# Kernel optimization log

Hardware: AMD Instinct MI355X
Metric: run time of the kernel (lower is better)

Reference implementation:

```python
import jax, jax.numpy as jnp
import numpy as np

C = 384
NH = 8        # LocalCrossAttention heads
CA_NH = 2     # inner CrossAttention heads
D_WIN = 6
SIGMA = D_WIN / 2.0
EPS = 1e-6


def _ln(x, g, b):
    mu = jnp.mean(x, axis=-1, keepdims=True)
    var = jnp.mean((x - mu) ** 2, axis=-1, keepdims=True)
    return (x - mu) / jnp.sqrt(var + EPS) * g + b


def _cross_attn(qx, kvx, Wq, Wkv, Wp, bp, nh):
    B, QN, c = qx.shape
    N = kvx.shape[1]
    hd = c // nh
    scale = hd ** -0.5
    qh = (qx @ Wq).reshape(B, QN, nh, hd).transpose(0, 2, 1, 3) * scale  # bhqd
    kvh = (kvx @ Wkv).reshape(B, N, 2, nh, hd).transpose(2, 0, 3, 1, 4)
    k, v = kvh[0], kvh[1]                                               # bhkd
    attn = jax.nn.softmax(jnp.einsum('bhqd,bhkd->bhqk', qh, k), axis=-1)
    x = jnp.einsum('bhqk,bhkd->bhqd', attn, v).transpose(0, 2, 1, 3).reshape(B, QN, c)
    return x @ Wp + bp


def _forward(q, kv, Wq, Wkv, Wproj, bproj, Wp_w, Wp_b, vp_w, vp_b, qpos_w, qpos_b,
             ca1_Wq, ca1_Wkv, ca1_Wproj, ca1_bproj,
             ca2_Wq, ca2_Wkv, ca2_Wproj, ca2_bproj,
             lnq1_g, lnq1_b, lnkv1_g, lnkv1_b, lnq2_g, lnq2_b, lnkv2_g, lnkv2_b, H, W):
    bs, QN, c = q.shape
    N = kv.shape[1]
    hd = c // NH
    scale = hd ** -0.5

    # main q/k/v
    qh = (q @ Wq).reshape(bs, QN, NH, hd).transpose(0, 2, 1, 3) * scale   # [bs,NH,QN,hd]
    kvh = (kv @ Wkv).reshape(bs, N, 2, NH, hd).transpose(2, 0, 3, 1, 4)
    k, v = kvh[0], kvh[1]                                                 # [bs,NH,N,hd]

    # position prediction branch
    q_for_pos = jnp.tile(q, (1, H, 1))                                    # [bs,QN*H,C]
    p = q_for_pos @ qpos_w + qpos_b
    p = _cross_attn(_ln(p, lnq1_g, lnq1_b), _ln(q_for_pos, lnkv1_g, lnkv1_b),
                    ca1_Wq, ca1_Wkv, ca1_Wproj, ca1_bproj, CA_NH)
    p = _cross_attn(_ln(p, lnq2_g, lnq2_b), _ln(kv, lnkv2_g, lnkv2_b),
                    ca2_Wq, ca2_Wkv, ca2_Wproj, ca2_bproj, CA_NH)
    p_t = jax.nn.sigmoid(jnp.tanh(p @ Wp_w + Wp_b) @ vp_w + vp_b) * W     # [bs,QN*H,1]

    # Gaussian window over W columns, broadcast over heads
    idx = jnp.arange(W, dtype=q.dtype)                                    # [W]
    gauss = jnp.exp(-((idx[None, :] - p_t) ** 2) / (2.0 * SIGMA ** 2))    # [bs,QN*H,W]
    gauss = gauss[:, None]                                                # [bs,1,QN*H,W]

    attn = jnp.einsum('bhqd,bhkd->bhqk', qh, k)                           # [bs,NH,QN,N]
    attn = attn.reshape(bs, NH, QN * H, W) * gauss
    attn = attn.reshape(bs, NH, QN, N)
    attn = jax.nn.softmax(attn, axis=-1)

    x = jnp.einsum('bhqk,bhkd->bhqd', attn, v).transpose(0, 2, 1, 3).reshape(bs, QN, c)
    return x @ Wproj + bproj


def setup_inputs() -> dict:
    key = jax.random.key(0)
    ks = jax.random.split(key, 16)
    s = 0.05
    d = {
        'q': jax.random.normal(ks[0], (32, 64, C), jnp.float32),
        'kv': jax.random.normal(ks[1], (32, 1024, C), jnp.float32),
        'Wq': jax.random.normal(ks[2], (C, C), jnp.float32) * s,
        'Wkv': jax.random.normal(ks[3], (C, 2 * C), jnp.float32) * s,
        'Wproj': jax.random.normal(ks[4], (C, C), jnp.float32) * s,
        'bproj': jnp.zeros((C,), jnp.float32),
        'Wp_w': jax.random.normal(ks[5], (C, C), jnp.float32) * s,
        'Wp_b': jnp.zeros((C,), jnp.float32),
        'vp_w': jax.random.normal(ks[6], (C, 1), jnp.float32) * s,
        'vp_b': jnp.zeros((1,), jnp.float32),
        'qpos_w': jax.random.normal(ks[7], (C, C), jnp.float32) * s,
        'qpos_b': jnp.zeros((C,), jnp.float32),
        'ca1_Wq': jax.random.normal(ks[8], (C, C), jnp.float32) * s,
        'ca1_Wkv': jax.random.normal(ks[9], (C, 2 * C), jnp.float32) * s,
        'ca1_Wproj': jax.random.normal(ks[10], (C, C), jnp.float32) * s,
        'ca1_bproj': jnp.zeros((C,), jnp.float32),
        'ca2_Wq': jax.random.normal(ks[11], (C, C), jnp.float32) * s,
        'ca2_Wkv': jax.random.normal(ks[12], (C, 2 * C), jnp.float32) * s,
        'ca2_Wproj': jax.random.normal(ks[13], (C, C), jnp.float32) * s,
        'ca2_bproj': jnp.zeros((C,), jnp.float32),
        'lnq1_g': jnp.ones((C,), jnp.float32), 'lnq1_b': jnp.zeros((C,), jnp.float32),
        'lnkv1_g': jnp.ones((C,), jnp.float32), 'lnkv1_b': jnp.zeros((C,), jnp.float32),
        'lnq2_g': jnp.ones((C,), jnp.float32), 'lnq2_b': jnp.zeros((C,), jnp.float32),
        'lnkv2_g': jnp.ones((C,), jnp.float32), 'lnkv2_b': jnp.zeros((C,), jnp.float32),
        'H': 8,
        'W': 128,
    }
    return d


def reference(q, kv, Wq, Wkv, Wproj, bproj, Wp_w, Wp_b, vp_w, vp_b, qpos_w, qpos_b,
              ca1_Wq, ca1_Wkv, ca1_Wproj, ca1_bproj,
              ca2_Wq, ca2_Wkv, ca2_Wproj, ca2_bproj,
              lnq1_g, lnq1_b, lnkv1_g, lnkv1_b, lnq2_g, lnq2_b, lnkv2_g, lnkv2_b, H, W):
    return _forward(q, kv, Wq, Wkv, Wproj, bproj, Wp_w, Wp_b, vp_w, vp_b, qpos_w, qpos_b,
                    ca1_Wq, ca1_Wkv, ca1_Wproj, ca1_bproj,
                    ca2_Wq, ca2_Wkv, ca2_Wproj, ca2_bproj,
                    lnq1_g, lnq1_b, lnkv1_g, lnkv1_b, lnq2_g, lnq2_b, lnkv2_g, lnkv2_b, H, W)
```

## Files before the change

kernel.cpp:

```cpp
#include <hip/hip_runtime.h>
#include <math.h>

#define MFMA __builtin_amdgcn_mfma_f32_16x16x32_bf16
typedef __attribute__((ext_vector_type(8))) short bf16x8;
typedef __attribute__((ext_vector_type(4))) float f32x4;
typedef unsigned short ushort_t;

__device__ __forceinline__ unsigned short tbf_hi(float x) {
    return (unsigned short)(__float_as_uint(x) >> 16);
}
__device__ __forceinline__ unsigned short tbf_lo(float x) {
    unsigned u = __float_as_uint(x);
    float r = x - __uint_as_float(u & 0xFFFF0000u);
    return (unsigned short)(__float_as_uint(r) >> 16);
}
__device__ __forceinline__ unsigned packhi(unsigned u0, unsigned u1) {
#if __has_builtin(__builtin_amdgcn_perm)
    return __builtin_amdgcn_perm(u1, u0, 0x07060302u);
#else
    return (u1 & 0xFFFF0000u) | (u0 >> 16);
#endif
}
__device__ __forceinline__ void tsplit8(const float* v, unsigned* hw, unsigned* lw) {
#pragma unroll
    for (int t = 0; t < 4; ++t) {
        unsigned u0 = __float_as_uint(v[2 * t]);
        unsigned u1 = __float_as_uint(v[2 * t + 1]);
        float r0 = v[2 * t]     - __uint_as_float(u0 & 0xFFFF0000u);
        float r1 = v[2 * t + 1] - __uint_as_float(u1 & 0xFFFF0000u);
        hw[t] = packhi(u0, u1);
        lw[t] = packhi(__float_as_uint(r0), __float_as_uint(r1));
    }
}

#if __has_builtin(__builtin_amdgcn_global_load_lds)
#define HAVE_GLDS 1
__device__ __forceinline__ void gld16(const ushort_t* g, ushort_t* l) {
    __builtin_amdgcn_global_load_lds(
        (const __attribute__((address_space(1))) unsigned int*)g,
        (__attribute__((address_space(3))) unsigned int*)l, 16, 0, 0);
}
#else
#define HAVE_GLDS 0
#endif

__global__ __launch_bounds__(256) void ln_stats_kernel(
    const float* __restrict__ src, float* __restrict__ mu,
    float* __restrict__ rs, int rows) {
    int row = blockIdx.x * 4 + (threadIdx.x >> 6);
    int lane = threadIdx.x & 63;
    if (row >= rows) return;
    const float* p = src + (size_t)row * 384;
    float s = 0.f, sq = 0.f;
#pragma unroll
    for (int i = 0; i < 6; ++i) {
        float v = p[lane + 64 * i];
        s += v; sq += v * v;
    }
#pragma unroll
    for (int off = 32; off > 0; off >>= 1) {
        s += __shfl_down(s, off);
        sq += __shfl_down(sq, off);
    }
    if (lane == 0) {
        float m = s / 384.f;
        float var = sq / 384.f - m * m;
        mu[row] = m;
        rs[row] = rsqrtf(var + 1e-6f);
    }
}

__global__ __launch_bounds__(256) void lnsplit_kernel(
    const float* __restrict__ src, float* __restrict__ mu,
    float* __restrict__ rs, ushort_t* __restrict__ dh,
    ushort_t* __restrict__ dl, int rows) {
    int row = blockIdx.x * 4 + (threadIdx.x >> 6);
    int lane = threadIdx.x & 63;
    if (row >= rows) return;
    const float* p = src + (size_t)row * 384;
    float v[6];
    float s = 0.f, sq = 0.f;
#pragma unroll
    for (int i = 0; i < 6; ++i) {
        v[i] = p[lane + 64 * i];
        s += v[i]; sq += v[i] * v[i];
    }
#pragma unroll
    for (int i = 0; i < 6; ++i) {
        dh[(size_t)row * 384 + lane + 64 * i] = tbf_hi(v[i]);
        dl[(size_t)row * 384 + lane + 64 * i] = tbf_lo(v[i]);
    }
#pragma unroll
    for (int off = 32; off > 0; off >>= 1) {
        s += __shfl_down(s, off);
        sq += __shfl_down(sq, off);
    }
    if (lane == 0) {
        float m = s / 384.f;
        float var = sq / 384.f - m * m;
        mu[row] = m;
        rs[row] = rsqrtf(var + 1e-6f);
    }
}

struct WprepTab {
    const float* src[10]; const float* g[10];
    ushort_t* dh[10]; ushort_t* dl[10];
    float scale[10]; int N[10];
};
__global__ __launch_bounds__(256) void wprep_all(WprepTab t) {
    int e = blockIdx.y;
    int N = t.N[e];
    int idx = blockIdx.x * 256 + threadIdx.x;
    if (idx >= N * 384) return;
    int n = idx / 384, k = idx % 384;
    float x = t.src[e][(size_t)k * N + n] * t.scale[e];
    if (t.g[e]) x *= t.g[e][k];
    t.dh[e][idx] = tbf_hi(x);
    t.dl[e][idx] = tbf_lo(x);
}

struct CmcbTab {
    const float* src[5]; const float* g[5]; const float* lb[5]; const float* badd[5];
    float* cm[5]; float* cb[5]; float scale[5]; int N[5];
};
__global__ __launch_bounds__(256) void cmcb_all(CmcbTab t) {
    int e = blockIdx.y;
    int N = t.N[e];
    int c = blockIdx.x * 4 + (threadIdx.x >> 6);
    int lane = threadIdx.x & 63;
    if (c >= N) return;
    float s1 = 0.f, s2 = 0.f;
    const float* gp = t.g[e];
#pragma unroll
    for (int i = 0; i < 6; ++i) {
        int k = lane + 64 * i;
        float w = t.src[e][(size_t)k * N + c];
        if (gp) s1 += gp[k] * w;
        s2 += t.lb[e][k] * w;
    }
#pragma unroll
    for (int off = 32; off > 0; off >>= 1) {
        s1 += __shfl_down(s1, off);
        s2 += __shfl_down(s2, off);
    }
    if (lane == 0) {
        if (t.cm[e]) t.cm[e][c] = -t.scale[e] * s1;
        float v = t.scale[e] * s2;
        if (t.badd[e]) v += t.badd[e][c];
        t.cb[e][c] = v;
    }
}

struct Slot {
    const float* bias; const float* cm; const float* cb;
    float* f32o; ushort_t* oh; ushort_t* ol;
    int mode; int kvsh;
};
struct GemmCfg { const float* muA; const float* rsA; Slot s[4]; };

template <int TM, int TN, int ASPLIT, int XSWZ>
__global__ __launch_bounds__(256) void gemm_k(
    const float* __restrict__ Af,
    const ushort_t* __restrict__ Ah, const ushort_t* __restrict__ Al,
    const ushort_t* __restrict__ Bh, const ushort_t* __restrict__ Bl,
    GemmCfg cfg) {
    constexpr int MI = TM / 64;
    constexpr int NI = TN / 16;
    constexpr int AR = TM / 32, BR = TN / 32;
    __shared__ __align__(16) ushort_t Alds[2][TM * 64];
    __shared__ __align__(16) ushort_t Blds[2][TN * 64];
    int bx = blockIdx.x, by = blockIdx.y;
    if (XSWZ) {
        int gx = gridDim.x;
        int nwg = gx * gridDim.y;
        int lin = by * gx + bx;
        int cpx = nwg >> 3;
        lin = (lin & 7) * cpx + (lin >> 3);
        by = lin / gx;
        bx = lin - by * gx;
    }
    int m0 = by * TM, n0 = bx * TN;
    int tid = threadIdx.x;
    int w = tid >> 6, lane = tid & 63;
    int j = lane & 15, kg = lane >> 4;
    int srow = tid >> 3, sk16 = tid & 7;
    f32x4 acc[MI][NI];
#pragma unroll
    for (int mi = 0; mi < MI; ++mi)
#pragma unroll
        for (int ni = 0; ni < NI; ++ni)
#pragma unroll
            for (int r = 0; r < 4; ++r) acc[mi][ni][r] = 0.f;

    for (int ks = 0; ks < 6; ++ks) {
        __syncthreads();
#if HAVE_GLDS
        if (ASPLIT) {
#pragma unroll
            for (int i = 0; i < TM / 32; ++i) {
                int lrow = w * (TM / 4) + i * 8 + (lane >> 3);
                int cc = (lane & 7) ^ (lrow & 7);
                size_t ga = (size_t)(m0 + lrow) * 384 + ks * 64 + cc * 8;
                ushort_t* d0 = &Alds[0][(w * (TM / 4) + i * 8) * 64];
                ushort_t* d1 = &Alds[1][(w * (TM / 4) + i * 8) * 64];
                gld16(Ah + ga, d0);
                gld16(Al + ga, d1);
            }
#pragma unroll
            for (int i = 0; i < TN / 32; ++i) {
                int lrow = w * (TN / 4) + i * 8 + (lane >> 3);
                int cc = (lane & 7) ^ (lrow & 7);
                size_t gb = (size_t)(n0 + lrow) * 384 + ks * 64 + cc * 8;
                ushort_t* d0 = &Blds[0][(w * (TN / 4) + i * 8) * 64];
                ushort_t* d1 = &Blds[1][(w * (TN / 4) + i * 8) * 64];
                gld16(Bh + gb, d0);
                gld16(Bl + gb, d1);
            }
        } else
#endif
        {
            int kbase = ks * 64 + sk16 * 8;
#pragma unroll
            for (int rnd = 0; rnd < AR; ++rnd) {
                int row = srow + rnd * 32;
                int off = (row << 6) + ((sk16 ^ (row & 7)) << 3);
                if (ASPLIT) {
                    size_t ga = (size_t)(m0 + row) * 384 + kbase;
                    *(bf16x8*)&Alds[0][off] = *(const bf16x8*)(Ah + ga);
                    *(bf16x8*)&Alds[1][off] = *(const bf16x8*)(Al + ga);
                } else {
                    const float* ap = Af + (size_t)(m0 + row) * 384 + kbase;
                    float v[8];
                    *(float4*)v = *(const float4*)ap;
                    *(float4*)(v + 4) = *(const float4*)(ap + 4);
                    unsigned hw[4], lw[4];
                    tsplit8(v, hw, lw);
                    *(uint4*)&Alds[0][off] = *(uint4*)hw;
                    *(uint4*)&Alds[1][off] = *(uint4*)lw;
                }
            }
#pragma unroll
            for (int rnd = 0; rnd < BR; ++rnd) {
                int row = srow + rnd * 32;
                int off = (row << 6) + ((sk16 ^ (row & 7)) << 3);
                size_t gb = (size_t)(n0 + row) * 384 + kbase;
                *(bf16x8*)&Blds[0][off] = *(const bf16x8*)(Bh + gb);
                *(bf16x8*)&Blds[1][off] = *(const bf16x8*)(Bl + gb);
            }
        }
        __syncthreads();
#pragma unroll
        for (int kf = 0; kf < 2; ++kf) {
            bf16x8 afh[MI], afl[MI], bfh[NI], bfl[NI];
#pragma unroll
            for (int mi = 0; mi < MI; ++mi) {
                int row = w * (TM / 4) + mi * 16 + j;
                int off = (row << 6) + ((((kf << 2) | kg) ^ (row & 7)) << 3);
                afh[mi] = *(const bf16x8*)&Alds[0][off];
                afl[mi] = *(const bf16x8*)&Alds[1][off];
            }
#pragma unroll
            for (int ni = 0; ni < NI; ++ni) {
                int col = ni * 16 + j;
                int off = (col << 6) + ((((kf << 2) | kg) ^ (col & 7)) << 3);
                bfh[ni] = *(const bf16x8*)&Blds[0][off];
                bfl[ni] = *(const bf16x8*)&Blds[1][off];
            }
#pragma unroll
            for (int mi = 0; mi < MI; ++mi)
#pragma unroll
                for (int ni = 0; ni < NI; ++ni) {
                    acc[mi][ni] = MFMA(afh[mi], bfh[ni], acc[mi][ni], 0, 0, 0);
                    acc[mi][ni] = MFMA(afh[mi], bfl[ni], acc[mi][ni], 0, 0, 0);
                    acc[mi][ni] = MFMA(afl[mi], bfh[ni], acc[mi][ni], 0, 0, 0);
                }
        }
    }
    int slot = n0 / 384;
    Slot sl = cfg.s[slot];
    int cb0 = n0 % 384;
#pragma unroll
    for (int mi = 0; mi < MI; ++mi)
#pragma unroll
        for (int ni = 0; ni < NI; ++ni)
#pragma unroll
            for (int r = 0; r < 4; ++r) {
                int row = m0 + w * (TM / 4) + mi * 16 + kg * 4 + r;
                int c2 = cb0 + ni * 16 + j;
                float v = acc[mi][ni][r];
                if (sl.cm) {
                    float rss = cfg.rsA[row];
                    v = rss * v + rss * cfg.muA[row] * sl.cm[c2] + sl.cb[c2];
                }
                if (sl.bias) v += sl.bias[c2];
                if (sl.mode == 0) {
                    sl.f32o[(size_t)row * 384 + c2] = v;
                } else if (sl.mode == 1) {
                    sl.f32o[(size_t)row * 384 + c2] = tanhf(v);
                } else if (sl.mode == 2) {
                    sl.oh[(size_t)row * 384 + c2] = tbf_hi(v);
                    sl.ol[(size_t)row * 384 + c2] = tbf_lo(v);
                } else if (sl.mode == 4) {
                    size_t o = (size_t)c2 * 384 + row;
                    sl.oh[o] = tbf_hi(v);
                    sl.ol[o] = tbf_lo(v);
                } else {
                    int bb = row >> sl.kvsh;
                    int key = row & ((1 << sl.kvsh) - 1);
                    size_t o = (((size_t)bb * 384 + c2) << sl.kvsh) + key;
                    sl.oh[o] = tbf_hi(v);
                    sl.ol[o] = tbf_lo(v);
                }
            }
}

template <int HD, int DPAD, int NW, int GAUSS, int FINAL>
__global__ __launch_bounds__(64 * NW) void attn_k(
    const ushort_t* __restrict__ Qh, const ushort_t* __restrict__ Ql,
    const ushort_t* __restrict__ Kh, const ushort_t* __restrict__ Kl,
    const ushort_t* __restrict__ Vth, const ushort_t* __restrict__ Vtl,
    const float* __restrict__ PT,
    ushort_t* __restrict__ Xh, ushort_t* __restrict__ Xl,
    float* __restrict__ Opart, float* __restrict__ ML,
    int kvsh, int nch, int NS, int nh) {
    constexpr int KS = DPAD / 32;
    constexpr int NSUB = HD / 16;
    constexpr int C8 = DPAD / 8;
    constexpr int NT = 64 * NW;
    __shared__ __align__(16) ushort_t Ksh[2][32][DPAD + 8];
    __shared__ __align__(16) ushort_t Vsh[2][HD][40];
    __shared__ __align__(16) ushort_t Psh[NW][2][16][40];
    __shared__ float ptbl[GAUSS ? 64 : 1];
    int b = blockIdx.z, h = blockIdx.y, chunk = blockIdx.x;
    int tid = threadIdx.x;
    int w = tid >> 6, lane = tid & 63;
    int l15 = lane & 15, kg = lane >> 4;

    bf16x8 qf[2][KS];
    {
        size_t qa = (size_t)(b * 64 + w * 16 + l15) * 384 + h * HD + kg * 8;
#pragma unroll
        for (int ks = 0; ks < KS; ++ks) {
            if (ks * 32 + kg * 8 < HD) {
                qf[0][ks] = *(const bf16x8*)(Qh + qa + ks * 32);
                qf[1][ks] = *(const bf16x8*)(Ql + qa + ks * 32);
            } else {
                qf[0][ks] = bf16x8{};
                qf[1][ks] = bf16x8{};
            }
        }
    }
    if (GAUSS) {
        if (tid < 64) ptbl[tid] = PT[b * 64 + tid];
    }
    f32x4 oacc[NSUB];
#pragma unroll
    for (int ns = 0; ns < NSUB; ++ns)
#pragma unroll
        for (int r = 0; r < 4; ++r) oacc[ns][r] = 0.f;
    float m_run[4], l_run[4];
#pragma unroll
    for (int r = 0; r < 4; ++r) { m_run[r] = -1e30f; l_run[r] = 0.f; }

    int kbase0 = chunk * nch;
    for (int t = 0; t < nch; t += 32) {
        int n0 = kbase0 + t;
        __syncthreads();
        for (int i = tid; i < 2 * 32 * C8; i += NT) {
            int hl = i / (32 * C8);
            int rem = i - hl * 32 * C8;
            int key = rem / C8, c = rem % C8;
            bf16x8 v;
            if (c * 8 < HD) {
                const ushort_t* src = (hl ? Kl : Kh) +
                    ((size_t)((b << kvsh) + n0 + key)) * 384 + h * HD + c * 8;
                v = *(const bf16x8*)src;
            } else {
                v = bf16x8{};
            }
            *(bf16x8*)&Ksh[hl][key][c * 8] = v;
        }
        for (int i = tid; i < 2 * HD * 4; i += NT) {
            int hl = i / (HD * 4);
            int rem = i - hl * HD * 4;
            int dim = rem >> 2, c = rem & 3;
            const ushort_t* src = (hl ? Vtl : Vth) +
                (((size_t)(b * 384 + h * HD + dim)) << kvsh) + n0 + c * 8;
            *(bf16x8*)&Vsh[hl][dim][c * 8] = *(const bf16x8*)src;
        }
        __syncthreads();

        f32x4 shh[2], slh[2], shl[2];
#pragma unroll
        for (int sub = 0; sub < 2; ++sub)
#pragma unroll
            for (int r = 0; r < 4; ++r) { shh[sub][r] = 0.f; slh[sub][r] = 0.f; shl[sub][r] = 0.f; }
#pragma unroll
        for (int sub = 0; sub < 2; ++sub)
#pragma unroll
            for (int ks = 0; ks < KS; ++ks) {
                bf16x8 kh8 = *(const bf16x8*)&Ksh[0][sub * 16 + l15][ks * 32 + kg * 8];
                bf16x8 kl8 = *(const bf16x8*)&Ksh[1][sub * 16 + l15][ks * 32 + kg * 8];
                shh[sub] = MFMA(qf[0][ks], kh8, shh[sub], 0, 0, 0);
                slh[sub] = MFMA(qf[1][ks], kh8, slh[sub], 0, 0, 0);
                shl[sub] = MFMA(qf[0][ks], kl8, shl[sub], 0, 0, 0);
            }
        f32x4 s[2];
#pragma unroll
        for (int sub = 0; sub < 2; ++sub)
#pragma unroll
            for (int r = 0; r < 4; ++r)
                s[sub][r] = shh[sub][r] + slh[sub][r] + shl[sub][r];
        if (GAUSS) {
            int win = n0 >> 7;
#pragma unroll
            for (int sub = 0; sub < 2; ++sub) {
                float wpos = (float)((n0 + sub * 16 + l15) & 127);
#pragma unroll
                for (int r = 0; r < 4; ++r) {
                    float ptv = ptbl[((w * 16 + kg * 4 + r) * 8 + win) & 63];
                    float d = wpos - ptv;
                    s[sub][r] *= __expf(d * d * (-1.0f / 18.0f));
                }
            }
        }
#pragma unroll
        for (int r = 0; r < 4; ++r) {
            float v = fmaxf(s[0][r], s[1][r]);
            v = fmaxf(v, __shfl_xor(v, 1));
            v = fmaxf(v, __shfl_xor(v, 2));
            v = fmaxf(v, __shfl_xor(v, 4));
            v = fmaxf(v, __shfl_xor(v, 8));
            float mnew = fmaxf(m_run[r], v);
            float alpha = __expf(m_run[r] - mnew);
            m_run[r] = mnew;
            float p0 = __expf(s[0][r] - mnew);
            float p1 = __expf(s[1][r] - mnew);
            float ps = p0 + p1;
            ps += __shfl_xor(ps, 1);
            ps += __shfl_xor(ps, 2);
            ps += __shfl_xor(ps, 4);
            ps += __shfl_xor(ps, 8);
            l_run[r] = l_run[r] * alpha + ps;
#pragma unroll
            for (int ns = 0; ns < NSUB; ++ns) oacc[ns][r] *= alpha;
            Psh[w][0][kg * 4 + r][l15] = tbf_hi(p0);
            Psh[w][1][kg * 4 + r][l15] = tbf_lo(p0);
            Psh[w][0][kg * 4 + r][16 + l15] = tbf_hi(p1);
            Psh[w][1][kg * 4 + r][16 + l15] = tbf_lo(p1);
        }
        bf16x8 pfh = *(const bf16x8*)&Psh[w][0][l15][kg * 8];
        bf16x8 pfl = *(const bf16x8*)&Psh[w][1][l15][kg * 8];
#pragma unroll
        for (int ns = 0; ns < NSUB; ++ns) {
            bf16x8 vh8 = *(const bf16x8*)&Vsh[0][ns * 16 + l15][kg * 8];
            bf16x8 vl8 = *(const bf16x8*)&Vsh[1][ns * 16 + l15][kg * 8];
            oacc[ns] = MFMA(pfh, vh8, oacc[ns], 0, 0, 0);
            oacc[ns] = MFMA(pfl, vh8, oacc[ns], 0, 0, 0);
            oacc[ns] = MFMA(pfh, vl8, oacc[ns], 0, 0, 0);
        }
    }
    if (FINAL) {
#pragma unroll
        for (int ns = 0; ns < NSUB; ++ns)
#pragma unroll
            for (int r = 0; r < 4; ++r) {
                float val = oacc[ns][r] / l_run[r];
                size_t o = (size_t)(b * 64 + w * 16 + kg * 4 + r) * 384 +
                           h * HD + ns * 16 + l15;
                Xh[o] = tbf_hi(val);
                Xl[o] = tbf_lo(val);
            }
    } else {
#pragma unroll
        for (int r = 0; r < 4; ++r) {
            int rq = w * 16 + kg * 4 + r;
            size_t Pidx = ((size_t)((b * nh + h) * 64 + rq)) * NS + chunk;
#pragma unroll
            for (int ns = 0; ns < NSUB; ++ns)
                Opart[Pidx * HD + ns * 16 + l15] = oacc[ns][r];
            if (l15 == 0) {
                ML[Pidx * 2] = m_run[r];
                ML[Pidx * 2 + 1] = l_run[r];
            }
        }
    }
}

template <int HD>
__global__ __launch_bounds__(256) void comb_k(
    const float* __restrict__ Opart, const float* __restrict__ ML,
    ushort_t* __restrict__ Xh, ushort_t* __restrict__ Xl,
    int NS, int nh) {
    int gw = blockIdx.x * 4 + (threadIdx.x >> 6);
    int lane = threadIdx.x & 63;
    if (gw >= 2048 * nh) return;
    int r_ = gw / nh, h = gw % nh;
    int b = r_ >> 6, rq = r_ & 63;
    size_t Pb = ((size_t)((b * nh + h) * 64 + rq)) * NS;
    float M = -1e30f;
    for (int c = 0; c < NS; ++c) M = fmaxf(M, ML[(Pb + c) * 2]);
    float wgt[8];
    float L = 0.f;
    for (int c = 0; c < NS; ++c) {
        wgt[c] = __expf(ML[(Pb + c) * 2] - M);
        L += wgt[c] * ML[(Pb + c) * 2 + 1];
    }
    float invL = 1.f / L;
    for (int d = lane; d < HD; d += 64) {
        float o = 0.f;
        for (int c = 0; c < NS; ++c) o += wgt[c] * Opart[(Pb + c) * HD + d];
        o *= invL;
        size_t xo = (size_t)r_ * 384 + h * HD + d;
        Xh[xo] = tbf_hi(o);
        Xl[xo] = tbf_lo(o);
    }
}

__global__ __launch_bounds__(256) void pt_kernel(
    const float* __restrict__ T, const float* __restrict__ vpw,
    const float* __restrict__ vpb, float* __restrict__ pt, int rows) {
    int row = blockIdx.x * 4 + (threadIdx.x >> 6);
    int lane = threadIdx.x & 63;
    if (row >= rows) return;
    const float* p = T + (size_t)row * 384;
    float s = 0.f;
#pragma unroll
    for (int i = 0; i < 6; ++i) s += p[lane + 64 * i] * vpw[lane + 64 * i];
#pragma unroll
    for (int off = 32; off > 0; off >>= 1) s += __shfl_down(s, off);
    if (lane == 0) {
        float x = s + vpb[0];
        pt[row] = 128.f / (1.f + __expf(-x));
    }
}

extern "C" void kernel_launch(void* const* d_in, const int* in_sizes, int n_in,
                              void* d_out, int out_size, void* d_ws, size_t ws_size,
                              hipStream_t stream) {
    const float* q       = (const float*)d_in[0];
    const float* kv      = (const float*)d_in[1];
    const float* Wq      = (const float*)d_in[2];
    const float* Wkv     = (const float*)d_in[3];
    const float* Wproj   = (const float*)d_in[4];
    const float* bproj   = (const float*)d_in[5];
    const float* Wp_w    = (const float*)d_in[6];
    const float* Wp_b    = (const float*)d_in[7];
    const float* vp_w    = (const float*)d_in[8];
    const float* vp_b    = (const float*)d_in[9];
    const float* qpos_w  = (const float*)d_in[10];
    const float* qpos_b  = (const float*)d_in[11];
    const float* ca1_Wq  = (const float*)d_in[12];
    const float* ca1_Wkv = (const float*)d_in[13];
    const float* ca1_Wp  = (const float*)d_in[14];
    const float* ca1_bp  = (const float*)d_in[15];
    const float* ca2_Wq  = (const float*)d_in[16];
    const float* ca2_Wkv = (const float*)d_in[17];
    const float* ca2_Wp  = (const float*)d_in[18];
    const float* ca2_bp  = (const float*)d_in[19];
    const float* lnq1_g  = (const float*)d_in[20];
    const float* lnq1_b  = (const float*)d_in[21];
    const float* lnkv1_g = (const float*)d_in[22];
    const float* lnkv1_b = (const float*)d_in[23];
    const float* lnq2_g  = (const float*)d_in[24];
    const float* lnq2_b  = (const float*)d_in[25];
    const float* lnkv2_g = (const float*)d_in[26];
    const float* lnkv2_b = (const float*)d_in[27];
    float* out = (float*)d_out;

    const float SC_CA = 0.07216878364870323f;
    const float SC_MA = 0.14433756729740643f;

    float* F = (float*)d_ws;
    float* R0 = F;    F += 786432;
    float* R1 = F;    F += 786432;
    float* MUq = F;   F += 2048;
    float* RSq = F;   F += 2048;
    float* MUkv = F;  F += 32768;
    float* RSkv = F;  F += 32768;
    float* MUpa = F;  F += 2048;
    float* RSpa = F;  F += 2048;
    float* MUpb = F;  F += 2048;
    float* RSpb = F;  F += 2048;
    float* PTb = F;   F += 2048;
    float* CM = F;    F += 2304;
    float* CB = F;    F += 2688;
    float* OP = F;    F += 6291456;
    float* MLb = F;   F += 262144;
    ushort_t* U = (ushort_t*)F;
    ushort_t* WB1h = U; U += 589824;
    ushort_t* WB1l = U; U += 589824;
    ushort_t* WB5h = U; U += 589824;
    ushort_t* WB5l = U; U += 589824;
    ushort_t* W2h = U;  U += 147456;
    ushort_t* W2l = U;  U += 147456;
    ushort_t* W3h = U;  U += 147456;
    ushort_t* W3l = U;  U += 147456;
    ushort_t* W4h = U;  U += 147456;
    ushort_t* W4l = U;  U += 147456;
    ushort_t* W67h = U; U += 147456;
    ushort_t* W67l = U; U += 147456;
    ushort_t* W7h = U;  U += 147456;
    ushort_t* W7l = U;  U += 147456;
    ushort_t* W10h = U; U += 147456;
    ushort_t* W10l = U; U += 147456;
    ushort_t* Qch = U;  U += 786432;
    ushort_t* Qcl = U;  U += 786432;
    ushort_t* Qmh = U;  U += 786432;
    ushort_t* Qml = U;  U += 786432;
    ushort_t* Xh = U;   U += 786432;
    ushort_t* Xl = U;   U += 786432;
    ushort_t* K1h = U;  U += 786432;
    ushort_t* K1l = U;  U += 786432;
    ushort_t* V1h = U;  U += 786432;
    ushort_t* V1l = U;  U += 786432;
    ushort_t* K2h = U;  U += 12582912;
    ushort_t* K2l = U;  U += 12582912;
    ushort_t* V2h = U;  U += 12582912;
    ushort_t* V2l = U;  U += 12582912;
    ushort_t* Qsh = U;  U += 786432;
    ushort_t* Qsl = U;  U += 786432;
    ushort_t* KVsh = U; U += 12582912;
    ushort_t* KVsl = U; U += 12582912;
    ushort_t* Kmh = K2h;
    ushort_t* Kml = K2l;
    ushort_t* Vmh = V2h;
    ushort_t* Vml = V2l;

    dim3 blk(256);

    lnsplit_kernel<<<512, blk, 0, stream>>>(q, MUq, RSq, Qsh, Qsl, 2048);
    lnsplit_kernel<<<8192, blk, 0, stream>>>(kv, MUkv, RSkv, KVsh, KVsl, 32768);

    WprepTab wt{};
    const float* wsrc[10] = {qpos_w, ca1_Wkv, Wq, ca2_Wkv, Wkv,
                             ca1_Wq, ca1_Wp, ca2_Wq, Wp_w, Wproj};
    const float* wg[10] = {nullptr, lnkv1_g, nullptr, lnkv2_g, nullptr,
                           lnq1_g, nullptr, lnq2_g, nullptr, nullptr};
    ushort_t* wdh[10] = {WB1h, WB1h + 384 * 384, WB1h + 1152 * 384,
                         WB5h, WB5h + 768 * 384, W2h, W3h, W4h, W7h, W10h};
    ushort_t* wdl[10] = {WB1l, WB1l + 384 * 384, WB1l + 1152 * 384,
                         WB5l, WB5l + 768 * 384, W2l, W3l, W4l, W7l, W10l};
    float wsc[10] = {1.f, 1.f, SC_MA, 1.f, 1.f, SC_CA, 1.f, SC_CA, 1.f, 1.f};
    int wn[10] = {384, 768, 384, 768, 768, 384, 384, 384, 384, 384};
    for (int i = 0; i < 10; ++i) {
        wt.src[i] = wsrc[i]; wt.g[i] = wg[i]; wt.dh[i] = wdh[i];
        wt.dl[i] = wdl[i]; wt.scale[i] = wsc[i]; wt.N[i] = wn[i];
    }
    wprep_all<<<dim3(1152, 10), blk, 0, stream>>>(wt);

    CmcbTab ct{};
    const float* csrc[5] = {ca1_Wq, ca1_Wkv, ca2_Wq, ca2_Wkv, Wp_w};
    const float* cg[5] = {lnq1_g, lnkv1_g, lnq2_g, lnkv2_g, nullptr};
    const float* cl[5] = {lnq1_b, lnkv1_b, lnq2_b, lnkv2_b, ca2_bp};
    const float* cbad[5] = {nullptr, nullptr, nullptr, nullptr, Wp_b};
    float* ccm[5] = {CM, CM + 384, CM + 1152, CM + 1536, nullptr};
    float* ccb[5] = {CB, CB + 384, CB + 1152, CB + 1536, CB + 2304};
    float csc[5] = {SC_CA, 1.f, SC_CA, 1.f, 1.f};
    int cn[5] = {384, 768, 384, 768, 384};
    for (int i = 0; i < 5; ++i) {
        ct.src[i] = csrc[i]; ct.g[i] = cg[i]; ct.lb[i] = cl[i]; ct.badd[i] = cbad[i];
        ct.cm[i] = ccm[i]; ct.cb[i] = ccb[i]; ct.scale[i] = csc[i]; ct.N[i] = cn[i];
    }
    cmcb_all<<<dim3(192, 5), blk, 0, stream>>>(ct);

    GemmCfg gW{};
    gW.s[0] = {nullptr, nullptr, nullptr, nullptr, W67h, W67l, 4, 0};
    gemm_k<64, 64, 0, 0><<<dim3(6, 6), blk, 0, stream>>>(ca2_Wp, nullptr, nullptr, W7h, W7l, gW);

    GemmCfg g5a{};
    g5a.muA = MUkv; g5a.rsA = RSkv;
    g5a.s[0] = {nullptr, CM + 1536, CB + 1536, nullptr, K2h, K2l, 2, 0};
    g5a.s[1] = {nullptr, CM + 1920, CB + 1920, nullptr, V2h, V2l, 3, 10};
    gemm_k<128, 64, 1, 1><<<dim3(12, 256), blk, 0, stream>>>(nullptr, KVsh, KVsl, WB5h, WB5l, g5a);

    GemmCfg g1{};
    g1.muA = MUq; g1.rsA = RSq;
    g1.s[0] = {qpos_b, nullptr, nullptr, R0, nullptr, nullptr, 0, 0};
    g1.s[1] = {nullptr, CM + 384, CB + 384, nullptr, K1h, K1l, 2, 0};
    g1.s[2] = {nullptr, CM + 768, CB + 768, nullptr, V1h, V1l, 3, 6};
    g1.s[3] = {nullptr, nullptr, nullptr, nullptr, Qmh, Qml, 2, 0};
    gemm_k<64, 64, 1, 1><<<dim3(24, 32), blk, 0, stream>>>(nullptr, Qsh, Qsl, WB1h, WB1l, g1);

    ln_stats_kernel<<<512, blk, 0, stream>>>(R0, MUpa, RSpa, 2048);

    GemmCfg g2{};
    g2.muA = MUpa; g2.rsA = RSpa;
    g2.s[0] = {nullptr, CM, CB, nullptr, Qch, Qcl, 2, 0};
    gemm_k<64, 64, 0, 0><<<dim3(6, 32), blk, 0, stream>>>(R0, nullptr, nullptr, W2h, W2l, g2);

    attn_k<192, 192, 4, 0, 1><<<dim3(1, 2, 32), blk, 0, stream>>>(
        Qch, Qcl, K1h, K1l, V1h, V1l, nullptr, Xh, Xl, nullptr, nullptr, 6, 64, 1, 2);

    GemmCfg g3{};
    g3.s[0] = {ca1_bp, nullptr, nullptr, R1, nullptr, nullptr, 0, 0};
    gemm_k<64, 64, 1, 0><<<dim3(6, 32), blk, 0, stream>>>(nullptr, Xh, Xl, W3h, W3l, g3);

    ln_stats_kernel<<<512, blk, 0, stream>>>(R1, MUpb, RSpb, 2048);

    GemmCfg g4{};
    g4.muA = MUpb; g4.rsA = RSpb;
    g4.s[0] = {nullptr, CM + 1152, CB + 1152, nullptr, Qch, Qcl, 2, 0};
    gemm_k<64, 64, 0, 0><<<dim3(6, 32), blk, 0, stream>>>(R1, nullptr, nullptr, W4h, W4l, g4);

    attn_k<192, 192, 4, 0, 0><<<dim3(8, 2, 32), blk, 0, stream>>>(
        Qch, Qcl, K2h, K2l, V2h, V2l, nullptr, nullptr, nullptr, OP, MLb, 10, 128, 8, 2);
    comb_k<192><<<1024, blk, 0, stream>>>(OP, MLb, Xh, Xl, 8, 2);

    GemmCfg g67{};
    g67.s[0] = {CB + 2304, nullptr, nullptr, R0, nullptr, nullptr, 1, 0};
    gemm_k<64, 64, 1, 0><<<dim3(6, 32), blk, 0, stream>>>(nullptr, Xh, Xl, W67h, W67l, g67);

    pt_kernel<<<512, blk, 0, stream>>>(R0, vp_w, vp_b, PTb, 2048);

    GemmCfg g5b{};
    g5b.s[0] = {nullptr, nullptr, nullptr, nullptr, Kmh, Kml, 2, 0};
    g5b.s[1] = {nullptr, nullptr, nullptr, nullptr, Vmh, Vml, 3, 10};
    gemm_k<128, 64, 1, 1><<<dim3(12, 256), blk, 0, stream>>>(nullptr, KVsh, KVsl,
        WB5h + 768 * 384, WB5l + 768 * 384, g5b);

    attn_k<48, 64, 4, 1, 0><<<dim3(8, 8, 32), blk, 0, stream>>>(
        Qmh, Qml, Kmh, Kml, Vmh, Vml, PTb, nullptr, nullptr, OP, MLb, 10, 128, 8, 8);
    comb_k<48><<<4096, blk, 0, stream>>>(OP, MLb, Xh, Xl, 8, 8);

    GemmCfg g10{};
    g10.s[0] = {bproj, nullptr, nullptr, out, nullptr, nullptr, 0, 0};
    gemm_k<64, 64, 1, 0><<<dim3(6, 32), blk, 0, stream>>>(nullptr, Xh, Xl, W10h, W10l, g10);
}
```

Before: 552.4 us.

## Double-buffer LDS in split-bf16 GEMM to overlap global loads with MFMA

For the ASPLIT path using direct global-to-LDS loads, the GEMM K loop now keeps two LDS buffers: it prefetches the next K slice into the alternate buffer and then waits with a partial vmcnt before computing on the current one. This is meant to hide global memory latency behind the MFMA work instead of serialising load, barrier and compute. The cost is twice the LDS footprint, which can lower occupancy. The hand-set vmcnt thresholds must match the exact number of issued loads, so other tile shapes carry a correctness risk.

```diff
diff --git a/kernel.cpp b/kernel.cpp
--- a/kernel.cpp
+++ b/kernel.cpp
@@ -168,8 +168,14 @@
     constexpr int MI = TM / 64;
     constexpr int NI = TN / 16;
     constexpr int AR = TM / 32, BR = TN / 32;
-    __shared__ __align__(16) ushort_t Alds[2][TM * 64];
-    __shared__ __align__(16) ushort_t Blds[2][TN * 64];
+#if HAVE_GLDS
+    constexpr int PIPE = ASPLIT;
+#else
+    constexpr int PIPE = 0;
+#endif
+    constexpr int NBUF = PIPE ? 2 : 1;
+    __shared__ __align__(16) ushort_t Alds[NBUF][2][TM * 64];
+    __shared__ __align__(16) ushort_t Blds[NBUF][2][TN * 64];
     int bx = blockIdx.x, by = blockIdx.y;
     if (XSWZ) {
         int gx = gridDim.x;
@@ -193,42 +199,93 @@
 #pragma unroll
             for (int r = 0; r < 4; ++r) acc[mi][ni][r] = 0.f;
 
-    for (int ks = 0; ks < 6; ++ks) {
-        __syncthreads();
 #if HAVE_GLDS
-        if (ASPLIT) {
-#pragma unroll
-            for (int i = 0; i < TM / 32; ++i) {
-                int lrow = w * (TM / 4) + i * 8 + (lane >> 3);
-                int cc = (lane & 7) ^ (lrow & 7);
-                size_t ga = (size_t)(m0 + lrow) * 384 + ks * 64 + cc * 8;
-                ushort_t* d0 = &Alds[0][(w * (TM / 4) + i * 8) * 64];
-                ushort_t* d1 = &Alds[1][(w * (TM / 4) + i * 8) * 64];
-                gld16(Ah + ga, d0);
-                gld16(Al + ga, d1);
-            }
-#pragma unroll
-            for (int i = 0; i < TN / 32; ++i) {
-                int lrow = w * (TN / 4) + i * 8 + (lane >> 3);
-                int cc = (lane & 7) ^ (lrow & 7);
-                size_t gb = (size_t)(n0 + lrow) * 384 + ks * 64 + cc * 8;
-                ushort_t* d0 = &Blds[0][(w * (TN / 4) + i * 8) * 64];
-                ushort_t* d1 = &Blds[1][(w * (TN / 4) + i * 8) * 64];
-                gld16(Bh + gb, d0);
-                gld16(Bl + gb, d1);
-            }
-        } else
+    auto stage = [&](int ks, int buf) {
+#pragma unroll
+        for (int i = 0; i < AR; ++i) {
+            int lrow = w * (TM / 4) + i * 8 + (lane >> 3);
+            int cc = (lane & 7) ^ (lrow & 7);
+            size_t ga = (size_t)(m0 + lrow) * 384 + ks * 64 + cc * 8;
+            gld16(Ah + ga, &Alds[buf][0][(w * (TM / 4) + i * 8) * 64]);
+            gld16(Al + ga, &Alds[buf][1][(w * (TM / 4) + i * 8) * 64]);
+        }
+#pragma unroll
+        for (int i = 0; i < BR; ++i) {
+            int lrow = w * (TN / 4) + i * 8 + (lane >> 3);
+            int cc = (lane & 7) ^ (lrow & 7);
+            size_t gb = (size_t)(n0 + lrow) * 384 + ks * 64 + cc * 8;
+            gld16(Bh + gb, &Blds[buf][0][(w * (TN / 4) + i * 8) * 64]);
+            gld16(Bl + gb, &Blds[buf][1][(w * (TN / 4) + i * 8) * 64]);
+        }
+    };
 #endif
-        {
+
+    auto compute = [&](int buf) {
+#pragma unroll
+        for (int kf = 0; kf < 2; ++kf) {
+            bf16x8 afh[MI], afl[MI], bfh[NI], bfl[NI];
+#pragma unroll
+            for (int mi = 0; mi < MI; ++mi) {
+                int row = w * (TM / 4) + mi * 16 + j;
+                int off = (row << 6) + ((((kf << 2) | kg) ^ (row & 7)) << 3);
+                afh[mi] = *(const bf16x8*)&Alds[buf][0][off];
+                afl[mi] = *(const bf16x8*)&Alds[buf][1][off];
+            }
+#pragma unroll
+            for (int ni = 0; ni < NI; ++ni) {
+                int col = ni * 16 + j;
+                int off = (col << 6) + ((((kf << 2) | kg) ^ (col & 7)) << 3);
+                bfh[ni] = *(const bf16x8*)&Blds[buf][0][off];
+                bfl[ni] = *(const bf16x8*)&Blds[buf][1][off];
+            }
+#pragma unroll
+            for (int mi = 0; mi < MI; ++mi)
+#pragma unroll
+                for (int ni = 0; ni < NI; ++ni) {
+                    acc[mi][ni] = MFMA(afh[mi], bfh[ni], acc[mi][ni], 0, 0, 0);
+                    acc[mi][ni] = MFMA(afh[mi], bfl[ni], acc[mi][ni], 0, 0, 0);
+                    acc[mi][ni] = MFMA(afl[mi], bfh[ni], acc[mi][ni], 0, 0, 0);
+                }
+        }
+    };
+
+#if HAVE_GLDS
+    if (PIPE) {
+        stage(0, 0);
+        int cur = 0;
+        for (int ks = 0; ks < 6; ++ks) {
+            if (ks < 5) {
+                stage(ks + 1, cur ^ 1);
+                if constexpr (2 * (AR + BR) == 12)
+                    asm volatile("s_waitcnt vmcnt(12)" ::: "memory");
+                else
+                    asm volatile("s_waitcnt vmcnt(8)" ::: "memory");
+            } else {
+                asm volatile("s_waitcnt vmcnt(0)" ::: "memory");
+            }
+            __builtin_amdgcn_s_barrier();
+            __builtin_amdgcn_sched_barrier(0);
+            compute(cur);
+            __builtin_amdgcn_sched_barrier(0);
+            asm volatile("s_waitcnt lgkmcnt(0)" ::: "memory");
+            __builtin_amdgcn_sched_barrier(0);
+            __builtin_amdgcn_s_barrier();
+            cur ^= 1;
+        }
+    } else
+#endif
+    {
+        for (int ks = 0; ks < 6; ++ks) {
             int kbase = ks * 64 + sk16 * 8;
+            __syncthreads();
 #pragma unroll
             for (int rnd = 0; rnd < AR; ++rnd) {
                 int row = srow + rnd * 32;
                 int off = (row << 6) + ((sk16 ^ (row & 7)) << 3);
                 if (ASPLIT) {
                     size_t ga = (size_t)(m0 + row) * 384 + kbase;
-                    *(bf16x8*)&Alds[0][off] = *(const bf16x8*)(Ah + ga);
-                    *(bf16x8*)&Alds[1][off] = *(const bf16x8*)(Al + ga);
+                    *(bf16x8*)&Alds[0][0][off] = *(const bf16x8*)(Ah + ga);
+                    *(bf16x8*)&Alds[0][1][off] = *(const bf16x8*)(Al + ga);
                 } else {
                     const float* ap = Af + (size_t)(m0 + row) * 384 + kbase;
                     float v[8];
@@ -236,8 +293,8 @@
                     *(float4*)(v + 4) = *(const float4*)(ap + 4);
                     unsigned hw[4], lw[4];
                     tsplit8(v, hw, lw);
-                    *(uint4*)&Alds[0][off] = *(uint4*)hw;
-                    *(uint4*)&Alds[1][off] = *(uint4*)lw;
+                    *(uint4*)&Alds[0][0][off] = *(uint4*)hw;
+                    *(uint4*)&Alds[0][1][off] = *(uint4*)lw;
                 }
             }
 #pragma unroll
@@ -245,38 +302,14 @@
                 int row = srow + rnd * 32;
                 int off = (row << 6) + ((sk16 ^ (row & 7)) << 3);
                 size_t gb = (size_t)(n0 + row) * 384 + kbase;
-                *(bf16x8*)&Blds[0][off] = *(const bf16x8*)(Bh + gb);
-                *(bf16x8*)&Blds[1][off] = *(const bf16x8*)(Bl + gb);
-            }
-        }
-        __syncthreads();
-#pragma unroll
-        for (int kf = 0; kf < 2; ++kf) {
-            bf16x8 afh[MI], afl[MI], bfh[NI], bfl[NI];
-#pragma unroll
-            for (int mi = 0; mi < MI; ++mi) {
-                int row = w * (TM / 4) + mi * 16 + j;
-                int off = (row << 6) + ((((kf << 2) | kg) ^ (row & 7)) << 3);
-                afh[mi] = *(const bf16x8*)&Alds[0][off];
-                afl[mi] = *(const bf16x8*)&Alds[1][off];
-            }
-#pragma unroll
-            for (int ni = 0; ni < NI; ++ni) {
-                int col = ni * 16 + j;
-                int off = (col << 6) + ((((kf << 2) | kg) ^ (col & 7)) << 3);
-                bfh[ni] = *(const bf16x8*)&Blds[0][off];
-                bfl[ni] = *(const bf16x8*)&Blds[1][off];
-            }
-#pragma unroll
-            for (int mi = 0; mi < MI; ++mi)
-#pragma unroll
-                for (int ni = 0; ni < NI; ++ni) {
-                    acc[mi][ni] = MFMA(afh[mi], bfh[ni], acc[mi][ni], 0, 0, 0);
-                    acc[mi][ni] = MFMA(afh[mi], bfl[ni], acc[mi][ni], 0, 0, 0);
-                    acc[mi][ni] = MFMA(afl[mi], bfh[ni], acc[mi][ni], 0, 0, 0);
-                }
-        }
-    }
+                *(bf16x8*)&Blds[0][0][off] = *(const bf16x8*)(Bh + gb);
+                *(bf16x8*)&Blds[0][1][off] = *(const bf16x8*)(Bl + gb);
+            }
+            __syncthreads();
+            compute(0);
+        }
+    }
+
     int slot = n0 / 384;
     Slot sl = cfg.s[slot];
     int cb0 = n0 % 384;
```

After: 690.0 us. 24.9% more time.

## Add 128x128 512-thread GEMM kernel with XCD swizzle for KV projections

Applied to the files above, without the earlier changes.

Adds a dedicated gemm_big kernel with 128x128 tiles and 8 waves. It replaces the 128x64 gemm_k launches for the two large KV projection GEMMs. The larger tile raises operand reuse from LDS, the block-index swizzle groups neighbouring tiles per XCD to improve L2 locality, and the transposed-V outputs are written as 4-wide vector stores. The trade-off is higher LDS use per block, 64 KB, and a grid of half as many blocks.

```diff
diff --git a/kernel.cpp b/kernel.cpp
--- a/kernel.cpp
+++ b/kernel.cpp
@@ -4,6 +4,7 @@
 #define MFMA __builtin_amdgcn_mfma_f32_16x16x32_bf16
 typedef __attribute__((ext_vector_type(8))) short bf16x8;
 typedef __attribute__((ext_vector_type(4))) float f32x4;
+typedef __attribute__((ext_vector_type(4))) unsigned short us4;
 typedef unsigned short ushort_t;
 
 __device__ __forceinline__ unsigned short tbf_hi(float x) {
@@ -202,20 +203,16 @@
                 int lrow = w * (TM / 4) + i * 8 + (lane >> 3);
                 int cc = (lane & 7) ^ (lrow & 7);
                 size_t ga = (size_t)(m0 + lrow) * 384 + ks * 64 + cc * 8;
-                ushort_t* d0 = &Alds[0][(w * (TM / 4) + i * 8) * 64];
-                ushort_t* d1 = &Alds[1][(w * (TM / 4) + i * 8) * 64];
-                gld16(Ah + ga, d0);
-                gld16(Al + ga, d1);
+                gld16(Ah + ga, &Alds[0][(w * (TM / 4) + i * 8) * 64]);
+                gld16(Al + ga, &Alds[1][(w * (TM / 4) + i * 8) * 64]);
             }
 #pragma unroll
             for (int i = 0; i < TN / 32; ++i) {
                 int lrow = w * (TN / 4) + i * 8 + (lane >> 3);
                 int cc = (lane & 7) ^ (lrow & 7);
                 size_t gb = (size_t)(n0 + lrow) * 384 + ks * 64 + cc * 8;
-                ushort_t* d0 = &Blds[0][(w * (TN / 4) + i * 8) * 64];
-                ushort_t* d1 = &Blds[1][(w * (TN / 4) + i * 8) * 64];
-                gld16(Bh + gb, d0);
-                gld16(Bl + gb, d1);
+                gld16(Bh + gb, &Blds[0][(w * (TN / 4) + i * 8) * 64]);
+                gld16(Bl + gb, &Blds[1][(w * (TN / 4) + i * 8) * 64]);
             }
         } else
 #endif
@@ -313,6 +310,124 @@
                     sl.ol[o] = tbf_lo(v);
                 }
             }
+}
+
+template <int XSWZ>
+__global__ __launch_bounds__(512, 4) void gemm_big(
+    const ushort_t* __restrict__ Ah, const ushort_t* __restrict__ Al,
+    const ushort_t* __restrict__ Bh, const ushort_t* __restrict__ Bl,
+    GemmCfg cfg) {
+    __shared__ __align__(16) ushort_t Alds[2][128 * 64];
+    __shared__ __align__(16) ushort_t Blds[2][128 * 64];
+    int bx = blockIdx.x, by = blockIdx.y;
+    if (XSWZ) {
+        int gx = gridDim.x;
+        int nwg = gx * gridDim.y;
+        int lin = by * gx + bx;
+        int cpx = nwg >> 3;
+        lin = (lin & 7) * cpx + (lin >> 3);
+        by = lin / gx;
+        bx = lin - by * gx;
+    }
+    int m0 = by * 128, n0 = bx * 128;
+    int tid = threadIdx.x;
+    int w = tid >> 6, lane = tid & 63;
+    int wm = w >> 2, wn = w & 3;
+    int j = lane & 15, kg = lane >> 4;
+    f32x4 acc[4][2];
+#pragma unroll
+    for (int mi = 0; mi < 4; ++mi)
+#pragma unroll
+        for (int ni = 0; ni < 2; ++ni)
+#pragma unroll
+            for (int r = 0; r < 4; ++r) acc[mi][ni][r] = 0.f;
+
+    for (int ks = 0; ks < 6; ++ks) {
+        __syncthreads();
+#pragma unroll
+        for (int i = 0; i < 2; ++i) {
+            int cbase = (i * 8 + w) * 64;
+            int chunk = cbase + lane;
+            int lrow = chunk >> 3;
+            int cc = (chunk & 7) ^ (lrow & 7);
+            size_t ga = (size_t)(m0 + lrow) * 384 + ks * 64 + cc * 8;
+            size_t gb = (size_t)(n0 + lrow) * 384 + ks * 64 + cc * 8;
+#if HAVE_GLDS
+            gld16(Ah + ga, &Alds[0][cbase * 8]);
+            gld16(Al + ga, &Alds[1][cbase * 8]);
+            gld16(Bh + gb, &Blds[0][cbase * 8]);
+            gld16(Bl + gb, &Blds[1][cbase * 8]);
+#else
+            *(bf16x8*)&Alds[0][chunk * 8] = *(const bf16x8*)(Ah + ga);
+            *(bf16x8*)&Alds[1][chunk * 8] = *(const bf16x8*)(Al + ga);
+            *(bf16x8*)&Blds[0][chunk * 8] = *(const bf16x8*)(Bh + gb);
+            *(bf16x8*)&Blds[1][chunk * 8] = *(const bf16x8*)(Bl + gb);
+#endif
+        }
+        __syncthreads();
+#pragma unroll
+        for (int kf = 0; kf < 2; ++kf) {
+            bf16x8 afh[4], afl[4], bfh[2], bfl[2];
+#pragma unroll
+            for (int mi = 0; mi < 4; ++mi) {
+                int row = wm * 64 + mi * 16 + j;
+                int off = (row << 6) + ((((kf << 2) | kg) ^ (row & 7)) << 3);
+                afh[mi] = *(const bf16x8*)&Alds[0][off];
+                afl[mi] = *(const bf16x8*)&Alds[1][off];
+            }
+#pragma unroll
+            for (int ni = 0; ni < 2; ++ni) {
+                int col = wn * 32 + ni * 16 + j;
+                int off = (col << 6) + ((((kf << 2) | kg) ^ (col & 7)) << 3);
+                bfh[ni] = *(const bf16x8*)&Blds[0][off];
+                bfl[ni] = *(const bf16x8*)&Blds[1][off];
+            }
+#pragma unroll
+            for (int mi = 0; mi < 4; ++mi)
+#pragma unroll
+                for (int ni = 0; ni < 2; ++ni) {
+                    acc[mi][ni] = MFMA(afh[mi], bfh[ni], acc[mi][ni], 0, 0, 0);
+                    acc[mi][ni] = MFMA(afh[mi], bfl[ni], acc[mi][ni], 0, 0, 0);
+                    acc[mi][ni] = MFMA(afl[mi], bfh[ni], acc[mi][ni], 0, 0, 0);
+                }
+        }
+    }
+    int slot = n0 / 384;
+    Slot sl = cfg.s[slot];
+    int cb0 = n0 % 384;
+#pragma unroll
+    for (int mi = 0; mi < 4; ++mi)
+#pragma unroll
+        for (int ni = 0; ni < 2; ++ni) {
+            int row0 = m0 + wm * 64 + mi * 16 + kg * 4;
+            int c2 = cb0 + wn * 32 + ni * 16 + j;
+            float v[4];
+#pragma unroll
+            for (int r = 0; r < 4; ++r) {
+                float x = acc[mi][ni][r];
+                if (sl.cm) {
+                    float rss = cfg.rsA[row0 + r];
+                    x = rss * x + rss * cfg.muA[row0 + r] * sl.cm[c2] + sl.cb[c2];
+                }
+                v[r] = x;
+            }
+            if (sl.mode == 2) {
+#pragma unroll
+                for (int r = 0; r < 4; ++r) {
+                    sl.oh[(size_t)(row0 + r) * 384 + c2] = tbf_hi(v[r]);
+                    sl.ol[(size_t)(row0 + r) * 384 + c2] = tbf_lo(v[r]);
+                }
+            } else {
+                int bb = row0 >> sl.kvsh;
+                int key = row0 & ((1 << sl.kvsh) - 1);
+                size_t o = (((size_t)bb * 384 + c2) << sl.kvsh) + key;
+                us4 h4, l4;
+#pragma unroll
+                for (int r = 0; r < 4; ++r) { h4[r] = tbf_hi(v[r]); l4[r] = tbf_lo(v[r]); }
+                *(us4*)(sl.oh + o) = h4;
+                *(us4*)(sl.ol + o) = l4;
+            }
+        }
 }
 
 template <int HD, int DPAD, int NW, int GAUSS, int FINAL>
@@ -673,7 +788,7 @@
     g5a.muA = MUkv; g5a.rsA = RSkv;
     g5a.s[0] = {nullptr, CM + 1536, CB + 1536, nullptr, K2h, K2l, 2, 0};
     g5a.s[1] = {nullptr, CM + 1920, CB + 1920, nullptr, V2h, V2l, 3, 10};
-    gemm_k<128, 64, 1, 1><<<dim3(12, 256), blk, 0, stream>>>(nullptr, KVsh, KVsl, WB5h, WB5l, g5a);
+    gemm_big<1><<<dim3(6, 256), dim3(512), 0, stream>>>(KVsh, KVsl, WB5h, WB5l, g5a);
 
     GemmCfg g1{};
     g1.muA = MUq; g1.rsA = RSq;
@@ -717,7 +832,7 @@
     GemmCfg g5b{};
     g5b.s[0] = {nullptr, nullptr, nullptr, nullptr, Kmh, Kml, 2, 0};
     g5b.s[1] = {nullptr, nullptr, nullptr, nullptr, Vmh, Vml, 3, 10};
-    gemm_k<128, 64, 1, 1><<<dim3(12, 256), blk, 0, stream>>>(nullptr, KVsh, KVsl,
+    gemm_big<1><<<dim3(6, 256), dim3(512), 0, stream>>>(KVsh, KVsl,
         WB5h + 768 * 384, WB5l + 768 * 384, g5b);
 
     attn_k<48, 64, 4, 1, 0><<<dim3(8, 8, 32), blk, 0, stream>>>(
```

Result: faster. 451.7 us (median of 2 runs) (-18.2%).
